# Performance work log

Hardware: AMD Instinct MI355X
Metric: run time of the kernel (lower is better)

## Reference

```python
import jax, jax.numpy as jnp
import numpy as np

N = 100_000   # num nodes
E = 1_600_000 # num edges
C = 128       # in_channels == hidden_channels
L = 3         # n_layers
EPS = 1e-5    # BatchNorm eps (torch default)


def bn(h, g, b, m, v):
    # BatchNorm1d in eval mode: running stats
    return (h - m) * jax.lax.rsqrt(v + EPS) * g + b


def sage_layer(h, src, dst, Wl_i, bl_i, Wr_i):
    # mean aggregation of incoming neighbor messages (PyG SAGEConv default)
    msg = h[src]                                                   # [E, C] gather
    agg = jax.ops.segment_sum(msg, dst, num_segments=N)            # [N, C]
    cnt = jax.ops.segment_sum(jnp.ones((src.shape[0],), h.dtype), dst, num_segments=N)
    agg = agg / jnp.maximum(cnt, 1.0)[:, None]
    return agg @ Wl_i + bl_i + h @ Wr_i                            # lin_l(agg) + lin_r(x)


def setup_inputs() -> dict:
    key = jax.random.key(0)
    ks = jax.random.split(key, 32)
    s = 0.05
    d = {}
    d["x"] = jax.random.normal(ks[0], (N, C), jnp.float32)
    d["edge_index"] = jax.random.randint(ks[1], (2, E), 0, N, dtype=jnp.int32)
    d["batch_size"] = 50_000
    d["Wl"] = jax.random.normal(ks[2], (L, C, C), jnp.float32) * s
    d["bl"] = jax.random.normal(ks[3], (L, C), jnp.float32) * s
    d["Wr"] = jax.random.normal(ks[4], (L, C, C), jnp.float32) * s
    d["bn_g"] = jax.random.uniform(ks[5], (L, C), jnp.float32, 0.5, 1.5)
    d["bn_b"] = jax.random.normal(ks[6], (L, C), jnp.float32) * s
    d["bn_m"] = jax.random.normal(ks[7], (L, C), jnp.float32) * s
    d["bn_v"] = jax.random.uniform(ks[8], (L, C), jnp.float32, 0.5, 1.5)
    d["cW1"] = jax.random.normal(ks[9], (C, C), jnp.float32) * s
    d["cb1"] = jax.random.normal(ks[10], (C,), jnp.float32) * s
    d["cg1"] = jax.random.uniform(ks[11], (C,), jnp.float32, 0.5, 1.5)
    d["cbe1"] = jax.random.normal(ks[12], (C,), jnp.float32) * s
    d["cm1"] = jax.random.normal(ks[13], (C,), jnp.float32) * s
    d["cv1"] = jax.random.uniform(ks[14], (C,), jnp.float32, 0.5, 1.5)
    d["cW2"] = jax.random.normal(ks[15], (C, C // 2), jnp.float32) * s
    d["cb2"] = jax.random.normal(ks[16], (C // 2,), jnp.float32) * s
    d["cg2"] = jax.random.uniform(ks[17], (C // 2,), jnp.float32, 0.5, 1.5)
    d["cbe2"] = jax.random.normal(ks[18], (C // 2,), jnp.float32) * s
    d["cm2"] = jax.random.normal(ks[19], (C // 2,), jnp.float32) * s
    d["cv2"] = jax.random.uniform(ks[20], (C // 2,), jnp.float32, 0.5, 1.5)
    d["cW3"] = jax.random.normal(ks[21], (C // 2, 1), jnp.float32) * s
    d["cb3"] = jax.random.normal(ks[22], (1,), jnp.float32) * s
    return d


def reference(x, edge_index, batch_size, Wl, bl, Wr, bn_g, bn_b, bn_m, bn_v,
              cW1, cb1, cg1, cbe1, cm1, cv1,
              cW2, cb2, cg2, cbe2, cm2, cv2, cW3, cb3):
    src, dst = edge_index[0], edge_index[1]
    h = x
    for l in range(L):  # small fixed layer count
        h = bn(jax.nn.relu(sage_layer(h, src, dst, Wl[l], bl[l], Wr[l])),
               bn_g[l], bn_b[l], bn_m[l], bn_v[l])
        # dropout is identity in eval mode
    h = h[:batch_size]                                             # [B, C] seed nodes
    h = jax.nn.relu(bn(h @ cW1 + cb1, cg1, cbe1, cm1, cv1))
    h = jax.nn.relu(bn(h @ cW2 + cb2, cg2, cbe2, cm2, cv2))
    return (h @ cW3 + cb3)[:, 0]                                   # [B]
```

## Files before the change

### kernel.cpp

```cpp
#include <hip/hip_runtime.h>

#define N_NODES 100000
#define N_EDGES 1600000
#define CDIM    128
#define BATCH   50000
#define NLAYERS 3
#define EPS_BN  1e-5f
#define LPAD    136

#define NBUCK   512
#define BW      196
#define EPB     4096
#define NEB     ((N_EDGES + EPB - 1) / EPB)
#define EBCAP   3584

#define ECAP    704

#define BBLK3   ((BATCH + 31) / 32)
#define L3ROWS  (BBLK3 * 32)

typedef __attribute__((ext_vector_type(8))) short short8;
typedef __attribute__((ext_vector_type(4))) float floatx4;
typedef __attribute__((ext_vector_type(2))) float floatx2;

__device__ __forceinline__ unsigned short f2bf(float f) {
    unsigned int u = __float_as_uint(f);
    u = u + 0x7FFFu + ((u >> 16) & 1u);
    return (unsigned short)(u >> 16);
}
__device__ __forceinline__ unsigned int pk2(float lo, float hi) {
    return (unsigned int)f2bf(lo) | ((unsigned int)f2bf(hi) << 16);
}

__device__ __forceinline__ floatx2 fp8x2_lo(unsigned int u) {
    return __builtin_amdgcn_cvt_pk_f32_fp8((int)u, false);
}
__device__ __forceinline__ floatx2 fp8x2_hi(unsigned int u) {
    return __builtin_amdgcn_cvt_pk_f32_fp8((int)u, true);
}
__device__ __forceinline__ unsigned int f32x4_to_fp8(float f0, float f1, float f2, float f3) {
    int w = __builtin_amdgcn_cvt_pk_fp8_f32(f0, f1, 0, false);
    w = __builtin_amdgcn_cvt_pk_fp8_f32(f2, f3, w, true);
    return (unsigned int)w;
}

__device__ __forceinline__ void acc8(uint2 u, floatx2& a01, floatx2& a23,
                                     floatx2& a45, floatx2& a67) {
    a01 = a01 + fp8x2_lo(u.x);
    a23 = a23 + fp8x2_hi(u.x);
    a45 = a45 + fp8x2_lo(u.y);
    a67 = a67 + fp8x2_hi(u.y);
}
__device__ __forceinline__ void acc8w(uint2 u, float w, floatx2& a01, floatx2& a23,
                                      floatx2& a45, floatx2& a67) {
    floatx2 wv; wv.x = w; wv.y = w;
    a01 = fp8x2_lo(u.x) * wv + a01;
    a23 = fp8x2_hi(u.x) * wv + a23;
    a45 = fp8x2_lo(u.y) * wv + a45;
    a67 = fp8x2_hi(u.y) * wv + a67;
}

#define OFF_HB0   6400000
#define OFF_HB1   12800000
#define OFF_SC    19200000
#define OFF_RP    19201152
#define OFF_BCNT  19301184
#define OFF_ELIST 19302752
#define OFF_EBUF  20902752
#define OFF_WCAT  22737760
#define OFF_WH1   22786912
#define OFF_WH2   22795104
#define OFF_XQ    22800000
#define OFF_HQ0   26000000
#define OFF_HQ1   29200000

#define CVX  2048
#define WBLK 384
#define HBLK 96
#define CONV_BLKS (CVX + WBLK + HBLK + 1)

__global__ __launch_bounds__(256) void convert_all(
        const float* __restrict__ x,
        const float* __restrict__ Wl, const float* __restrict__ Wr,
        const float* __restrict__ cW1, const float* __restrict__ cW2,
        const float* __restrict__ g, const float* __restrict__ b,
        const float* __restrict__ m, const float* __restrict__ v,
        const float* __restrict__ cg1, const float* __restrict__ cbe1,
        const float* __restrict__ cm1, const float* __restrict__ cv1,
        const float* __restrict__ cg2, const float* __restrict__ cbe2,
        const float* __restrict__ cm2, const float* __restrict__ cv2,
        float* __restrict__ ws) {
    int blk = blockIdx.x;
    int tid = threadIdx.x;
    unsigned short* xb = (unsigned short*)ws;

    if (blk < CVX) {
        const int total = N_NODES * CDIM / 4;
        unsigned int* xq = (unsigned int*)(ws + OFF_XQ);
        for (int i = blk * 256 + tid; i < total; i += CVX * 256) {
            float4 vv = ((const float4*)x)[i];
            ushort4 o;
            o.x = f2bf(vv.x); o.y = f2bf(vv.y); o.z = f2bf(vv.z); o.w = f2bf(vv.w);
            ((ushort4*)xb)[i] = o;
            xq[i] = f32x4_to_fp8(vv.x, vv.y, vv.z, vv.w);
        }
        return;
    }
    if (blk < CVX + WBLK) {
        unsigned short* wcat = (unsigned short*)(ws + OFF_WCAT);
        int i = (blk - CVX) * 256 + tid;
        int l = i >> 15;
        int n = (i >> 8) & 127;
        int k = i & 255;
        float w = (k < CDIM) ? Wl[((size_t)l * CDIM + k) * CDIM + n]
                             : Wr[((size_t)l * CDIM + (k - CDIM)) * CDIM + n];
        wcat[i] = f2bf(w);
        return;
    }
    if (blk < CVX + WBLK + HBLK) {
        unsigned short* wh1 = (unsigned short*)(ws + OFF_WH1);
        unsigned short* wh2 = (unsigned short*)(ws + OFF_WH2);
        int i = (blk - CVX - WBLK) * 256 + tid;
        if (i < 128 * 128) {
            int n = i >> 7, k = i & 127;
            wh1[i] = f2bf(cW1[k * 128 + n]);
        } else if (i < 128 * 128 + 64 * 128) {
            int j = i - 128 * 128;
            int n = j >> 7, k = j & 127;
            wh2[j] = f2bf(cW2[k * 64 + n]);
        }
        return;
    }
    float* sc = ws + OFF_SC;
    for (int i = tid; i < NLAYERS * CDIM; i += 256) {
        float s = g[i] * rsqrtf(v[i] + EPS_BN);
        sc[i] = s;
        sc[NLAYERS * CDIM + i] = b[i] - m[i] * s;
    }
    if (tid < CDIM) {
        float s = cg1[tid] * rsqrtf(cv1[tid] + EPS_BN);
        sc[768 + tid] = s;
        sc[896 + tid] = cbe1[tid] - cm1[tid] * s;
    }
    if (tid < 64) {
        float s = cg2[tid] * rsqrtf(cv2[tid] + EPS_BN);
        sc[1024 + tid] = s;
        sc[1088 + tid] = cbe2[tid] - cm2[tid] * s;
    }
}

__global__ __launch_bounds__(256) void bucket_fill(const int* __restrict__ ei,
                                                   int* __restrict__ bcnt,
                                                   unsigned int* __restrict__ ebuf) {
    __shared__ unsigned int st[EPB];
    __shared__ unsigned short sb[EPB];
    __shared__ int lh[NBUCK];
    __shared__ int gb[NBUCK];
    __shared__ int lc[NBUCK];
    int tid = threadIdx.x;
    for (int t = tid; t < NBUCK; t += 256) { lh[t] = 0; lc[t] = 0; }
    __syncthreads();
    int base = blockIdx.x * EPB;
    int cnt = min(EPB, N_EDGES - base);
    for (int k = tid; k < cnt / 4; k += 256) {
        int4 s4 = ((const int4*)(ei + base))[k];
        int4 d4 = ((const int4*)(ei + N_EDGES + base))[k];
        int i0 = k * 4;
#pragma unroll
        for (int q = 0; q < 4; ++q) {
            int s = (q == 0) ? s4.x : (q == 1) ? s4.y : (q == 2) ? s4.z : s4.w;
            int d = (q == 0) ? d4.x : (q == 1) ? d4.y : (q == 2) ? d4.z : d4.w;
            int bk = (unsigned)d / BW;
            int ld = d - bk * BW;
            st[i0 + q] = (unsigned)s | ((unsigned)ld << 17);
            sb[i0 + q] = (unsigned short)bk;
            atomicAdd(&lh[bk], 1);
        }
    }
    __syncthreads();
    for (int t = tid; t < NBUCK; t += 256) {
        int c = lh[t];
        gb[t] = c ? (t * EBCAP + atomicAdd(&bcnt[t], c)) : 0;
    }
    __syncthreads();
    for (int i = tid; i < cnt; i += 256) {
        int bk = sb[i];
        int pos = gb[bk] + atomicAdd(&lc[bk], 1);
        ebuf[pos] = st[i];
    }
}

__global__ __launch_bounds__(256) void bucket_csr(const unsigned int* __restrict__ ebuf,
                                                  const int* __restrict__ bcnt,
                                                  int* __restrict__ elist,
                                                  int* __restrict__ rowptr) {
    __shared__ int sbb[NBUCK];
    __shared__ unsigned int st[EBCAP];
    __shared__ int out[EBCAP];
    __shared__ int h[256], sscan[256], pre[256], cur[256];
    int b = blockIdx.x;
    int tid = threadIdx.x;
    int cnt = min(bcnt[b], EBCAP);

    sbb[tid] = bcnt[tid];
    sbb[tid + 256] = bcnt[tid + 256];
    h[tid] = 0; cur[tid] = 0;
    __syncthreads();
    for (int off = 1; off < NBUCK; off <<= 1) {
        int v0 = (tid >= off) ? sbb[tid - off] : 0;
        int t2 = tid + 256;
        int v1 = sbb[t2 - off];
        __syncthreads();
        sbb[tid] += v0;
        sbb[t2] += v1;
        __syncthreads();
    }
    int obase = (b == 0) ? 0 : sbb[b - 1];

    int ebase = b * EBCAP;
    for (int i = tid; i < cnt; i += 256) {
        unsigned int u = ebuf[ebase + i];
        st[i] = u;
        atomicAdd(&h[u >> 17], 1);
    }
    __syncthreads();
    sscan[tid] = h[tid];
    __syncthreads();
    for (int off = 1; off < 256; off <<= 1) {
        int v = (tid >= off) ? sscan[tid - off] : 0;
        __syncthreads();
        sscan[tid] += v;
        __syncthreads();
    }
    pre[tid] = sscan[tid] - h[tid];
    __syncthreads();
    for (int i = tid; i < cnt; i += 256) {
        unsigned int u = st[i];
        int ld = u >> 17;
        int pos = pre[ld] + atomicAdd(&cur[ld], 1);
        out[pos] = (int)(u & 0x1FFFFu);
    }
    __syncthreads();
    for (int i = tid; i < cnt; i += 256) elist[obase + i] = out[i];
    int gn = b * BW + tid;
    if (tid < BW && gn < N_NODES) rowptr[gn] = obase + pre[tid];
    if (b == 0 && tid == 0) rowptr[N_NODES] = N_EDGES;
}

__global__ __launch_bounds__(256, 6) void sage_fused(const int* __restrict__ rowptr,
                                                     const int* __restrict__ elist,
                                                     const unsigned short* __restrict__ hin,
                                                     const unsigned char* __restrict__ hinq,
                                                     unsigned short* __restrict__ hout,
                                                     unsigned char* __restrict__ houtq,
                                                     int wq,
                                                     int bf16_limit,
                                                     const unsigned short* __restrict__ wcat,
                                                     const float* __restrict__ bl,
                                                     const float* __restrict__ scale,
                                                     const float* __restrict__ shift,
                                                     const unsigned short* __restrict__ wh1,
                                                     const unsigned short* __restrict__ wh2,
                                                     const float* __restrict__ cb1,
                                                     const float* __restrict__ s1,
                                                     const float* __restrict__ t1,
                                                     const float* __restrict__ cb2,
                                                     const float* __restrict__ s2,
                                                     const float* __restrict__ t2,
                                                     const float* __restrict__ W3,
                                                     const float* __restrict__ b3,
                                                     float* __restrict__ out) {
    __shared__ unsigned short sA[32][LPAD];
    __shared__ unsigned short sH[32][LPAD];
    __shared__ int selist[ECAP + 8];
    __shared__ int srp[33];
    __shared__ float sP[4][32];
    __shared__ float sw3[64];

    int row0 = blockIdx.x * 32;
    int tid = threadIdx.x;
    int lane = tid & 31;
    int grp = tid >> 5;
    int sub = lane >> 4;
    int li  = lane & 15;
    int li8 = li * 8;

    int beg0 = rowptr[row0];
    int end0 = rowptr[row0 + 32];
    int ecnt = min(end0 - beg0, ECAP);
    for (int i = tid; i < ecnt + 8; i += 256)
        selist[i] = (i < ecnt) ? elist[beg0 + i] : 0;
    if (tid < 33) srp[tid] = rowptr[row0 + tid];
    if (out && tid < 64) sw3[tid] = W3[tid];
    for (int it = 0; it < 4; ++it) {
        int idx = it * 256 + tid;
        int r = idx >> 5;
        int c4 = idx & 31;
        uint2 u = ((const uint2*)(hin + (size_t)(row0 + r) * CDIM))[c4];
        *((uint2*)&sH[r][c4 * 4]) = u;
    }
    __syncthreads();

    for (int rr = 0; rr < 4; ++rr) {
        int r = rr * 8 + grp;
        int beg = srp[r];
        int end = srp[r + 1];
        bool all_cached = (end - beg0) <= ecnt;
        floatx2 a01 = (floatx2)0.f, a23 = (floatx2)0.f,
                a45 = (floatx2)0.f, a67 = (floatx2)0.f;

        for (int j = beg + sub * 8; j < end; j += 16) {
            int lj = j - beg0;
            int s0, s1q, s2q, s3q, s4q, s5q, s6q, s7q;
            if (all_cached || (lj + 8 <= ecnt)) {
                s0  = selist[lj];     s1q = selist[lj + 1];
                s2q = selist[lj + 2]; s3q = selist[lj + 3];
                s4q = selist[lj + 4]; s5q = selist[lj + 5];
                s6q = selist[lj + 6]; s7q = selist[lj + 7];
            } else {
                s0  = elist[j];     s1q = elist[j + 1];
                s2q = elist[j + 2]; s3q = elist[j + 3];
                s4q = elist[j + 4]; s5q = elist[j + 5];
                s6q = elist[j + 6]; s7q = elist[j + 7];
            }
            bool p1 = (j + 1 < end), p2 = (j + 2 < end), p3 = (j + 3 < end),
                 p4 = (j + 4 < end), p5 = (j + 5 < end), p6 = (j + 6 < end),
                 p7 = (j + 7 < end);
            s1q = p1 ? s1q : 0; s2q = p2 ? s2q : 0; s3q = p3 ? s3q : 0;
            s4q = p4 ? s4q : 0; s5q = p5 ? s5q : 0; s6q = p6 ? s6q : 0;
            s7q = p7 ? s7q : 0;
            uint2 u0 = *((const uint2*)(hinq + (unsigned)((s0  << 7) + li8)));
            uint2 u1 = *((const uint2*)(hinq + (unsigned)((s1q << 7) + li8)));
            uint2 u2 = *((const uint2*)(hinq + (unsigned)((s2q << 7) + li8)));
            uint2 u3 = *((const uint2*)(hinq + (unsigned)((s3q << 7) + li8)));
            uint2 u4 = *((const uint2*)(hinq + (unsigned)((s4q << 7) + li8)));
            uint2 u5 = *((const uint2*)(hinq + (unsigned)((s5q << 7) + li8)));
            uint2 u6 = *((const uint2*)(hinq + (unsigned)((s6q << 7) + li8)));
            uint2 u7 = *((const uint2*)(hinq + (unsigned)((s7q << 7) + li8)));
            acc8(u0, a01, a23, a45, a67);
            acc8w(u1, p1 ? 1.f : 0.f, a01, a23, a45, a67);
            acc8w(u2, p2 ? 1.f : 0.f, a01, a23, a45, a67);
            acc8w(u3, p3 ? 1.f : 0.f, a01, a23, a45, a67);
            acc8w(u4, p4 ? 1.f : 0.f, a01, a23, a45, a67);
            acc8w(u5, p5 ? 1.f : 0.f, a01, a23, a45, a67);
            acc8w(u6, p6 ? 1.f : 0.f, a01, a23, a45, a67);
            acc8w(u7, p7 ? 1.f : 0.f, a01, a23, a45, a67);
        }

        float a0 = a01.x, a1 = a01.y, a2 = a23.x, a3 = a23.y,
              a4 = a45.x, a5 = a45.y, a6 = a67.x, a7 = a67.y;
        a0 += __shfl_xor(a0, 16); a1 += __shfl_xor(a1, 16);
        a2 += __shfl_xor(a2, 16); a3 += __shfl_xor(a3, 16);
        a4 += __shfl_xor(a4, 16); a5 += __shfl_xor(a5, 16);
        a6 += __shfl_xor(a6, 16); a7 += __shfl_xor(a7, 16);
        if (sub == 0) {
            float rin = 1.0f / fmaxf((float)(end - beg), 1.0f);
            uint4 o;
            o.x = pk2(a0 * rin, a1 * rin);
            o.y = pk2(a2 * rin, a3 * rin);
            o.z = pk2(a4 * rin, a5 * rin);
            o.w = pk2(a6 * rin, a7 * rin);
            *((uint4*)&sA[r][li8]) = o;
        }
    }
    __syncthreads();

    int wave = tid >> 6;
    int wl   = tid & 63;
    int ln16 = wl & 15;
    int quad = wl >> 4;

    floatx4 acc[2][2];
#pragma unroll
    for (int mt = 0; mt < 2; ++mt)
#pragma unroll
        for (int nt = 0; nt < 2; ++nt) acc[mt][nt] = (floatx4)0.0f;

    const unsigned short* wbase = wcat + ((size_t)(wave * 32 + ln16) * 256 + quad * 8);

#pragma unroll
    for (int kb = 0; kb < 8; ++kb) {
        int koff = (kb & 3) * 32 + quad * 8;
        const unsigned short* sbuf = (kb < 4) ? &sA[0][0] : &sH[0][0];
        short8 a0 = *((const short8*)(sbuf + (ln16)      * LPAD + koff));
        short8 a1 = *((const short8*)(sbuf + (ln16 + 16) * LPAD + koff));
        short8 b0 = *((const short8*)(wbase + kb * 32));
        short8 b1 = *((const short8*)(wbase + 16 * 256 + kb * 32));
        acc[0][0] = __builtin_amdgcn_mfma_f32_16x16x32_bf16(a0, b0, acc[0][0], 0, 0, 0);
        acc[1][0] = __builtin_amdgcn_mfma_f32_16x16x32_bf16(a1, b0, acc[1][0], 0, 0, 0);
        acc[0][1] = __builtin_amdgcn_mfma_f32_16x16x32_bf16(a0, b1, acc[0][1], 0, 0, 0);
        acc[1][1] = __builtin_amdgcn_mfma_f32_16x16x32_bf16(a1, b1, acc[1][1], 0, 0, 0);
    }

    __syncthreads();
#pragma unroll
    for (int nt = 0; nt < 2; ++nt) {
        int col = wave * 32 + nt * 16 + ln16;
        float bb = bl[col];
        float ss = scale[col];
        float tt = shift[col];
#pragma unroll
        for (int mt = 0; mt < 2; ++mt) {
#pragma unroll
            for (int r = 0; r < 4; ++r) {
                float v = fmaxf(acc[mt][nt][r] + bb, 0.0f) * ss + tt;
                sA[mt * 16 + quad * 4 + r][col] = f2bf(v);
            }
        }
    }
    __syncthreads();

    if (!out) {
#pragma unroll
        for (int it = 0; it < 2; ++it) {
            int idx = it * 256 + tid;
            int r = idx >> 4;
            int c = idx & 15;
            uint4 u = *((const uint4*)&sA[r][c * 8]);
            if (row0 + r < bf16_limit)
                *((uint4*)(hout + (size_t)(row0 + r) * CDIM + c * 8)) = u;
            if (wq) {
                float f0 = __uint_as_float(u.x << 16), f1 = __uint_as_float(u.x & 0xFFFF0000u);
                float f2 = __uint_as_float(u.y << 16), f3 = __uint_as_float(u.y & 0xFFFF0000u);
                float f4 = __uint_as_float(u.z << 16), f5 = __uint_as_float(u.z & 0xFFFF0000u);
                float f6 = __uint_as_float(u.w << 16), f7 = __uint_as_float(u.w & 0xFFFF0000u);
                uint2 q;
                q.x = f32x4_to_fp8(f0, f1, f2, f3);
                q.y = f32x4_to_fp8(f4, f5, f6, f7);
                *((uint2*)(houtq + (size_t)(row0 + r) * 128 + c * 8)) = q;
            }
        }
        return;
    }

    floatx4 h1[2][2];
#pragma unroll
    for (int mt = 0; mt < 2; ++mt) { h1[mt][0] = (floatx4)0.0f; h1[mt][1] = (floatx4)0.0f; }
    const unsigned short* w1a = wh1 + (size_t)(wave * 32 + ln16) * 128 + quad * 8;
    const unsigned short* w1b = w1a + 16 * 128;
#pragma unroll
    for (int kb = 0; kb < 4; ++kb) {
        int koff = kb * 32 + quad * 8;
        short8 b0 = *((const short8*)(w1a + kb * 32));
        short8 b1 = *((const short8*)(w1b + kb * 32));
#pragma unroll
        for (int mt = 0; mt < 2; ++mt) {
            short8 af = *((const short8*)(&sA[mt * 16 + ln16][koff]));
            h1[mt][0] = __builtin_amdgcn_mfma_f32_16x16x32_bf16(af, b0, h1[mt][0], 0, 0, 0);
            h1[mt][1] = __builtin_amdgcn_mfma_f32_16x16x32_bf16(af, b1, h1[mt][1], 0, 0, 0);
        }
    }
    __syncthreads();
#pragma unroll
    for (int nt = 0; nt < 2; ++nt) {
        int col = wave * 32 + nt * 16 + ln16;
        float bb = cb1[col], ss = s1[col], tt = t1[col];
#pragma unroll
        for (int mt = 0; mt < 2; ++mt) {
#pragma unroll
            for (int r = 0; r < 4; ++r) {
                float v = fmaxf((h1[mt][nt][r] + bb) * ss + tt, 0.0f);
                sA[mt * 16 + quad * 4 + r][col] = f2bf(v);
            }
        }
    }
    __syncthreads();

    floatx4 h2[2];
    h2[0] = (floatx4)0.0f; h2[1] = (floatx4)0.0f;
    const unsigned short* w2a = wh2 + (size_t)(wave * 16 + ln16) * 128 + quad * 8;
#pragma unroll
    for (int kb = 0; kb < 4; ++kb) {
        int koff = kb * 32 + quad * 8;
        short8 b0 = *((const short8*)(w2a + kb * 32));
#pragma unroll
        for (int mt = 0; mt < 2; ++mt) {
            short8 af = *((const short8*)(&sA[mt * 16 + ln16][koff]));
            h2[mt] = __builtin_amdgcn_mfma_f32_16x16x32_bf16(af, b0, h2[mt], 0, 0, 0);
        }
    }
    {
        int col = wave * 16 + ln16;
        float bb = cb2[col], ss = s2[col], tt = t2[col];
        float w3v = sw3[col];
#pragma unroll
        for (int mt = 0; mt < 2; ++mt) {
#pragma unroll
            for (int r = 0; r < 4; ++r) {
                float v = fmaxf((h2[mt][r] + bb) * ss + tt, 0.0f) * w3v;
                v += __shfl_xor(v, 1);
                v += __shfl_xor(v, 2);
                v += __shfl_xor(v, 4);
                v += __shfl_xor(v, 8);
                if (ln16 == 0) sP[wave][mt * 16 + quad * 4 + r] = v;
            }
        }
    }
    __syncthreads();
    if (tid < 32) {
        int row = row0 + tid;
        if (row < BATCH)
            out[row] = sP[0][tid] + sP[1][tid] + sP[2][tid] + sP[3][tid] + b3[0];
    }
}

extern "C" void kernel_launch(void* const* d_in, const int* in_sizes, int n_in,
                              void* d_out, int out_size, void* d_ws, size_t ws_size,
                              hipStream_t stream) {
    const float* x    = (const float*)d_in[0];
    const int*   ei   = (const int*)d_in[1];
    const float* Wl   = (const float*)d_in[3];
    const float* bl   = (const float*)d_in[4];
    const float* Wr   = (const float*)d_in[5];
    const float* bn_g = (const float*)d_in[6];
    const float* bn_b = (const float*)d_in[7];
    const float* bn_m = (const float*)d_in[8];
    const float* bn_v = (const float*)d_in[9];
    const float* cW1  = (const float*)d_in[10];
    const float* cb1  = (const float*)d_in[11];
    const float* cg1  = (const float*)d_in[12];
    const float* cbe1 = (const float*)d_in[13];
    const float* cm1  = (const float*)d_in[14];
    const float* cv1  = (const float*)d_in[15];
    const float* cW2  = (const float*)d_in[16];
    const float* cb2  = (const float*)d_in[17];
    const float* cg2  = (const float*)d_in[18];
    const float* cbe2 = (const float*)d_in[19];
    const float* cm2  = (const float*)d_in[20];
    const float* cv2  = (const float*)d_in[21];
    const float* cW3  = (const float*)d_in[22];
    const float* cb3  = (const float*)d_in[23];

    float* ws  = (float*)d_ws;
    unsigned short* xb  = (unsigned short*)ws;
    unsigned short* hb0 = (unsigned short*)(ws + OFF_HB0);
    unsigned short* hb1 = (unsigned short*)(ws + OFF_HB1);
    float* sc    = ws + OFF_SC;
    int* rowptr  = (int*)(ws + OFF_RP);
    int* bcnt    = (int*)(ws + OFF_BCNT);
    int* elist   = (int*)(ws + OFF_ELIST);
    unsigned int* ebuf = (unsigned int*)(ws + OFF_EBUF);
    unsigned short* wcat = (unsigned short*)(ws + OFF_WCAT);
    unsigned short* wh1  = (unsigned short*)(ws + OFF_WH1);
    unsigned short* wh2  = (unsigned short*)(ws + OFF_WH2);
    unsigned char* xq  = (unsigned char*)(ws + OFF_XQ);
    unsigned char* hq0 = (unsigned char*)(ws + OFF_HQ0);
    unsigned char* hq1 = (unsigned char*)(ws + OFF_HQ1);

    hipMemsetAsync(bcnt, 0, NBUCK * sizeof(int), stream);

    convert_all<<<CONV_BLKS, 256, 0, stream>>>(
        x, Wl, Wr, cW1, cW2,
        bn_g, bn_b, bn_m, bn_v,
        cg1, cbe1, cm1, cv1,
        cg2, cbe2, cm2, cv2, ws);

    bucket_fill<<<NEB, 256, 0, stream>>>(ei, bcnt, ebuf);
    bucket_csr<<<NBUCK, 256, 0, stream>>>(ebuf, bcnt, elist, rowptr);

    sage_fused<<<N_NODES / 32, 256, 0, stream>>>(
        rowptr, elist, xb, xq, hb0, hq0, 1, N_NODES,
        wcat, bl, sc, sc + 384,
        nullptr, nullptr, nullptr, nullptr, nullptr,
        nullptr, nullptr, nullptr, nullptr, nullptr, nullptr);
    sage_fused<<<N_NODES / 32, 256, 0, stream>>>(
        rowptr, elist, hb0, hq0, hb1, hq1, 1, L3ROWS,
        wcat + (size_t)CDIM * 256, bl + CDIM, sc + CDIM, sc + 384 + CDIM,
        nullptr, nullptr, nullptr, nullptr, nullptr,
        nullptr, nullptr, nullptr, nullptr, nullptr, nullptr);
    sage_fused<<<BBLK3, 256, 0, stream>>>(
        rowptr, elist, hb1, hq1, hb0, hq0, 0, 0,
        wcat + (size_t)2 * CDIM * 256, bl + 2 * CDIM, sc + 2 * CDIM, sc + 384 + 2 * CDIM,
        wh1, wh2,
        cb1, sc + 768, sc + 896,
        cb2, sc + 1024, sc + 1088,
        cW3, cb3, (float*)d_out);
}
```

Measured before the change: 331.2 us.

## Split bucket fill into count and deterministic scatter with coalesced bucket writes

Replaces the single atomic-offset bucket_fill with two passes. A count pass records per-block bucket histograms, and a scatter pass computes exclusive offsets by summing the histograms of preceding blocks. The scatter pass also sorts edges by bucket in shared memory before writing, so global stores to each bucket are contiguous and ordered deterministically. The cost is an extra kernel launch, a second read of the destination indices, and a serial prefix loop over up to 391 blocks per thread in the scatter kernel.

```diff
diff --git a/kernel.cpp b/kernel.cpp
--- a/kernel.cpp
+++ b/kernel.cpp
@@ -73,6 +73,7 @@
 #define OFF_XQ    22800000
 #define OFF_HQ0   26000000
 #define OFF_HQ1   29200000
+#define OFF_CNT2  32400000
 
 #define CVX  2048
 #define WBLK 384
@@ -149,18 +150,55 @@
     }
 }
 
-__global__ __launch_bounds__(256) void bucket_fill(const int* __restrict__ ei,
-                                                   int* __restrict__ bcnt,
-                                                   unsigned int* __restrict__ ebuf) {
+__global__ __launch_bounds__(256) void bucket_count(const int* __restrict__ ei,
+                                                    int* __restrict__ cnt2d,
+                                                    int* __restrict__ bcnt) {
+    __shared__ int lh[NBUCK];
+    int tid = threadIdx.x;
+    for (int t = tid; t < NBUCK; t += 256) lh[t] = 0;
+    __syncthreads();
+    int base = blockIdx.x * EPB;
+    int cnt = min(EPB, N_EDGES - base);
+    for (int k = tid; k < cnt / 4; k += 256) {
+        int4 d4 = ((const int4*)(ei + N_EDGES + base))[k];
+        atomicAdd(&lh[(unsigned)d4.x / BW], 1);
+        atomicAdd(&lh[(unsigned)d4.y / BW], 1);
+        atomicAdd(&lh[(unsigned)d4.z / BW], 1);
+        atomicAdd(&lh[(unsigned)d4.w / BW], 1);
+    }
+    __syncthreads();
+    for (int t = tid; t < NBUCK; t += 256) {
+        int c = lh[t];
+        cnt2d[blockIdx.x * NBUCK + t] = c;
+        if (c) atomicAdd(&bcnt[t], c);
+    }
+}
+
+__global__ __launch_bounds__(256) void bucket_scatter(const int* __restrict__ ei,
+                                                      const int* __restrict__ cnt2d,
+                                                      unsigned int* __restrict__ ebuf) {
     __shared__ unsigned int st[EPB];
     __shared__ unsigned short sb[EPB];
-    __shared__ int lh[NBUCK];
-    __shared__ int gb[NBUCK];
-    __shared__ int lc[NBUCK];
+    __shared__ unsigned int st2[EPB];
+    __shared__ unsigned short sb2[EPB];
+    __shared__ int lh[NBUCK], lsc[NBUCK], lc[NBUCK];
+    __shared__ int soff[NBUCK];
+    int blk = blockIdx.x;
     int tid = threadIdx.x;
+
+    {
+        int off0 = 0, off1 = 0;
+        for (int j = 0; j < blk; ++j) {
+            off0 += cnt2d[j * NBUCK + tid];
+            off1 += cnt2d[j * NBUCK + tid + 256];
+        }
+        soff[tid] = off0;
+        soff[tid + 256] = off1;
+    }
     for (int t = tid; t < NBUCK; t += 256) { lh[t] = 0; lc[t] = 0; }
     __syncthreads();
-    int base = blockIdx.x * EPB;
+
+    int base = blk * EPB;
     int cnt = min(EPB, N_EDGES - base);
     for (int k = tid; k < cnt / 4; k += 256) {
         int4 s4 = ((const int4*)(ei + base))[k];
@@ -178,15 +216,31 @@
         }
     }
     __syncthreads();
-    for (int t = tid; t < NBUCK; t += 256) {
-        int c = lh[t];
-        gb[t] = c ? (t * EBCAP + atomicAdd(&bcnt[t], c)) : 0;
-    }
-    __syncthreads();
+    lsc[tid] = lh[tid];
+    lsc[tid + 256] = lh[tid + 256];
+    __syncthreads();
+    for (int off = 1; off < NBUCK; off <<= 1) {
+        int v0 = (tid >= off) ? lsc[tid - off] : 0;
+        int t2 = tid + 256;
+        int v1 = lsc[t2 - off];
+        __syncthreads();
+        lsc[tid] += v0;
+        lsc[t2] += v1;
+        __syncthreads();
+    }
     for (int i = tid; i < cnt; i += 256) {
         int bk = sb[i];
-        int pos = gb[bk] + atomicAdd(&lc[bk], 1);
-        ebuf[pos] = st[i];
+        int r = atomicAdd(&lc[bk], 1);
+        int p = lsc[bk] - lh[bk] + r;
+        st2[p] = st[i];
+        sb2[p] = (unsigned short)bk;
+    }
+    __syncthreads();
+    for (int i = tid; i < cnt; i += 256) {
+        int bk = sb2[i];
+        int rank = i - (lsc[bk] - lh[bk]);
+        int g = soff[bk] + rank;
+        if (g < EBCAP) ebuf[bk * EBCAP + g] = st2[i];
     }
 }
 
@@ -546,6 +600,7 @@
     unsigned char* xq  = (unsigned char*)(ws + OFF_XQ);
     unsigned char* hq0 = (unsigned char*)(ws + OFF_HQ0);
     unsigned char* hq1 = (unsigned char*)(ws + OFF_HQ1);
+    int* cnt2d = (int*)(ws + OFF_CNT2);
 
     hipMemsetAsync(bcnt, 0, NBUCK * sizeof(int), stream);
 
@@ -555,7 +610,8 @@
         cg1, cbe1, cm1, cv1,
         cg2, cbe2, cm2, cv2, ws);
 
-    bucket_fill<<<NEB, 256, 0, stream>>>(ei, bcnt, ebuf);
+    bucket_count<<<NEB, 256, 0, stream>>>(ei, cnt2d, bcnt);
+    bucket_scatter<<<NEB, 256, 0, stream>>>(ei, cnt2d, ebuf);
     bucket_csr<<<NBUCK, 256, 0, stream>>>(ebuf, bcnt, elist, rowptr);
 
     sage_fused<<<N_NODES / 32, 256, 0, stream>>>(
```

New measurement: 384.2 us. +16.0%, slower.

## Split bucket fill into count, offset scan, and scatter passes fused with conversion

Applied to the files above, without the earlier changes.

Replaces the single bucket_fill kernel, which used global atomics for bucket offsets, with a three-phase scheme. The per-block bucket histogram is folded into the conversion kernel, a per-bucket scan produces deterministic offsets, and a scatter kernel writes edges directly. This also removes the memset and shrinks the x-conversion grid so the counting overlaps with conversion. In exchange it adds an extra kernel launch and reads the edge destinations twice.

```diff
diff --git a/kernel.cpp b/kernel.cpp
--- a/kernel.cpp
+++ b/kernel.cpp
@@ -73,13 +73,15 @@
 #define OFF_XQ    22800000
 #define OFF_HQ0   26000000
 #define OFF_HQ1   29200000
-
-#define CVX  2048
+#define OFF_CNT2  32400000
+#define OFF_BOFF  32600192
+
+#define CVX  512
 #define WBLK 384
 #define HBLK 96
-#define CONV_BLKS (CVX + WBLK + HBLK + 1)
-
-__global__ __launch_bounds__(256) void convert_all(
+#define CC_BLKS (NEB + CVX + WBLK + HBLK + 1)
+
+__global__ __launch_bounds__(256) void conv_count(
         const float* __restrict__ x,
         const float* __restrict__ Wl, const float* __restrict__ Wr,
         const float* __restrict__ cW1, const float* __restrict__ cW2,
@@ -89,15 +91,36 @@
         const float* __restrict__ cm1, const float* __restrict__ cv1,
         const float* __restrict__ cg2, const float* __restrict__ cbe2,
         const float* __restrict__ cm2, const float* __restrict__ cv2,
+        const int* __restrict__ ei,
+        int* __restrict__ cnt2d,
         float* __restrict__ ws) {
+    __shared__ int lh[NBUCK];
     int blk = blockIdx.x;
     int tid = threadIdx.x;
     unsigned short* xb = (unsigned short*)ws;
 
-    if (blk < CVX) {
+    if (blk < NEB) {
+        for (int t = tid; t < NBUCK; t += 256) lh[t] = 0;
+        __syncthreads();
+        int base = blk * EPB;
+        int cnt = min(EPB, N_EDGES - base);
+        for (int k = tid; k < cnt / 4; k += 256) {
+            int4 d4 = ((const int4*)(ei + N_EDGES + base))[k];
+            atomicAdd(&lh[(unsigned)d4.x / BW], 1);
+            atomicAdd(&lh[(unsigned)d4.y / BW], 1);
+            atomicAdd(&lh[(unsigned)d4.z / BW], 1);
+            atomicAdd(&lh[(unsigned)d4.w / BW], 1);
+        }
+        __syncthreads();
+        for (int t = tid; t < NBUCK; t += 256)
+            cnt2d[blk * NBUCK + t] = lh[t];
+        return;
+    }
+    int cb = blk - NEB;
+    if (cb < CVX) {
         const int total = N_NODES * CDIM / 4;
         unsigned int* xq = (unsigned int*)(ws + OFF_XQ);
-        for (int i = blk * 256 + tid; i < total; i += CVX * 256) {
+        for (int i = cb * 256 + tid; i < total; i += CVX * 256) {
             float4 vv = ((const float4*)x)[i];
             ushort4 o;
             o.x = f2bf(vv.x); o.y = f2bf(vv.y); o.z = f2bf(vv.z); o.w = f2bf(vv.w);
@@ -106,9 +129,10 @@
         }
         return;
     }
-    if (blk < CVX + WBLK) {
+    cb -= CVX;
+    if (cb < WBLK) {
         unsigned short* wcat = (unsigned short*)(ws + OFF_WCAT);
-        int i = (blk - CVX) * 256 + tid;
+        int i = cb * 256 + tid;
         int l = i >> 15;
         int n = (i >> 8) & 127;
         int k = i & 255;
@@ -117,10 +141,11 @@
         wcat[i] = f2bf(w);
         return;
     }
-    if (blk < CVX + WBLK + HBLK) {
+    cb -= WBLK;
+    if (cb < HBLK) {
         unsigned short* wh1 = (unsigned short*)(ws + OFF_WH1);
         unsigned short* wh2 = (unsigned short*)(ws + OFF_WH2);
-        int i = (blk - CVX - WBLK) * 256 + tid;
+        int i = cb * 256 + tid;
         if (i < 128 * 128) {
             int n = i >> 7, k = i & 127;
             wh1[i] = f2bf(cW1[k * 128 + n]);
@@ -149,44 +174,58 @@
     }
 }
 
-__global__ __launch_bounds__(256) void bucket_fill(const int* __restrict__ ei,
-                                                   int* __restrict__ bcnt,
-                                                   unsigned int* __restrict__ ebuf) {
-    __shared__ unsigned int st[EPB];
-    __shared__ unsigned short sb[EPB];
-    __shared__ int lh[NBUCK];
-    __shared__ int gb[NBUCK];
+__global__ __launch_bounds__(256) void bucket_offsets(const int* __restrict__ cnt2d,
+                                                      int* __restrict__ boff,
+                                                      int* __restrict__ bcnt) {
+    __shared__ int s[512];
+    int b = blockIdx.x;
+    int tid = threadIdx.x;
+    int i1 = tid + 256;
+    int v0 = (tid < NEB) ? cnt2d[tid * NBUCK + b] : 0;
+    int v1 = (i1 < NEB) ? cnt2d[i1 * NBUCK + b] : 0;
+    s[tid] = v0;
+    s[i1] = v1;
+    __syncthreads();
+    for (int off = 1; off < 512; off <<= 1) {
+        int a0 = (tid >= off) ? s[tid - off] : 0;
+        int a1 = s[i1 - off];
+        __syncthreads();
+        s[tid] += a0;
+        s[i1] += a1;
+        __syncthreads();
+    }
+    if (tid < NEB) boff[tid * NBUCK + b] = s[tid] - v0;
+    if (i1 < NEB) boff[i1 * NBUCK + b] = s[i1] - v1;
+    if (tid == 0) bcnt[b] = s[NEB - 1];
+}
+
+__global__ __launch_bounds__(256) void bucket_scatter(const int* __restrict__ ei,
+                                                      const int* __restrict__ boff,
+                                                      unsigned int* __restrict__ ebuf) {
+    __shared__ int soff[NBUCK];
     __shared__ int lc[NBUCK];
+    int blk = blockIdx.x;
     int tid = threadIdx.x;
-    for (int t = tid; t < NBUCK; t += 256) { lh[t] = 0; lc[t] = 0; }
-    __syncthreads();
-    int base = blockIdx.x * EPB;
+    soff[tid] = boff[blk * NBUCK + tid];
+    soff[tid + 256] = boff[blk * NBUCK + tid + 256];
+    lc[tid] = 0; lc[tid + 256] = 0;
+    __syncthreads();
+    int base = blk * EPB;
     int cnt = min(EPB, N_EDGES - base);
     for (int k = tid; k < cnt / 4; k += 256) {
         int4 s4 = ((const int4*)(ei + base))[k];
         int4 d4 = ((const int4*)(ei + N_EDGES + base))[k];
-        int i0 = k * 4;
 #pragma unroll
         for (int q = 0; q < 4; ++q) {
             int s = (q == 0) ? s4.x : (q == 1) ? s4.y : (q == 2) ? s4.z : s4.w;
             int d = (q == 0) ? d4.x : (q == 1) ? d4.y : (q == 2) ? d4.z : d4.w;
             int bk = (unsigned)d / BW;
             int ld = d - bk * BW;
-            st[i0 + q] = (unsigned)s | ((unsigned)ld << 17);
-            sb[i0 + q] = (unsigned short)bk;
-            atomicAdd(&lh[bk], 1);
-        }
-    }
-    __syncthreads();
-    for (int t = tid; t < NBUCK; t += 256) {
-        int c = lh[t];
-        gb[t] = c ? (t * EBCAP + atomicAdd(&bcnt[t], c)) : 0;
-    }
-    __syncthreads();
-    for (int i = tid; i < cnt; i += 256) {
-        int bk = sb[i];
-        int pos = gb[bk] + atomicAdd(&lc[bk], 1);
-        ebuf[pos] = st[i];
+            int r = atomicAdd(&lc[bk], 1);
+            int gpos = soff[bk] + r;
+            if (gpos < EBCAP)
+                ebuf[bk * EBCAP + gpos] = (unsigned)s | ((unsigned)ld << 17);
+        }
     }
 }
 
@@ -546,16 +585,18 @@
     unsigned char* xq  = (unsigned char*)(ws + OFF_XQ);
     unsigned char* hq0 = (unsigned char*)(ws + OFF_HQ0);
     unsigned char* hq1 = (unsigned char*)(ws + OFF_HQ1);
-
-    hipMemsetAsync(bcnt, 0, NBUCK * sizeof(int), stream);
-
-    convert_all<<<CONV_BLKS, 256, 0, stream>>>(
+    int* cnt2d = (int*)(ws + OFF_CNT2);
+    int* boff  = (int*)(ws + OFF_BOFF);
+
+    conv_count<<<CC_BLKS, 256, 0, stream>>>(
         x, Wl, Wr, cW1, cW2,
         bn_g, bn_b, bn_m, bn_v,
         cg1, cbe1, cm1, cv1,
-        cg2, cbe2, cm2, cv2, ws);
-
-    bucket_fill<<<NEB, 256, 0, stream>>>(ei, bcnt, ebuf);
+        cg2, cbe2, cm2, cv2,
+        ei, cnt2d, ws);
+
+    bucket_offsets<<<NBUCK, 256, 0, stream>>>(cnt2d, boff, bcnt);
+    bucket_scatter<<<NEB, 256, 0, stream>>>(ei, boff, ebuf);
     bucket_csr<<<NBUCK, 256, 0, stream>>>(ebuf, bcnt, elist, rowptr);
 
     sage_fused<<<N_NODES / 32, 256, 0, stream>>>(
```

New measurement: 341.9 us. 1.03x slower.
